# Kernel tuning notes

Measured on AMD Instinct MI355X. Metric: run time of the kernel, lower is better.

The kernel has to match this reference:

```python
import jax, jax.numpy as jnp
import numpy as np

E = 128  # embed_size


def setup_inputs() -> dict:
    key = jax.random.key(0)
    ks = jax.random.split(key, 20)
    NU, NI, NEV = 100000, 50000, 4096
    s = 0.05  # weight scale so softplus(dot) stays well-conditioned
    inp = {
        "user_emb": jax.random.normal(ks[0], (NU, E), jnp.float32) * s,
        "item_emb": jax.random.normal(ks[1], (NI, E), jnp.float32) * s,
        "ugru_wi": jax.random.normal(ks[2], (3 * E, E), jnp.float32) * s,
        "ugru_wh": jax.random.normal(ks[3], (3 * E, E), jnp.float32) * s,
        "ugru_bi": jax.random.normal(ks[4], (3 * E,), jnp.float32) * s,
        "ugru_bh": jax.random.normal(ks[5], (3 * E,), jnp.float32) * s,
        "igru_wi": jax.random.normal(ks[6], (3 * E, E), jnp.float32) * s,
        "igru_wh": jax.random.normal(ks[7], (3 * E, E), jnp.float32) * s,
        "igru_bi": jax.random.normal(ks[8], (3 * E,), jnp.float32) * s,
        "igru_bh": jax.random.normal(ks[9], (3 * E,), jnp.float32) * s,
        "t1_w": jax.random.normal(ks[10], (E, 2 * E), jnp.float32) * s,
        "t1_b": jax.random.normal(ks[11], (E,), jnp.float32) * s,
        "t2_w": jax.random.normal(ks[12], (32, E), jnp.float32) * s,
        "t2_b": jax.random.normal(ks[13], (32,), jnp.float32) * s,
        "t3_w": jax.random.normal(ks[14], (1, 32), jnp.float32) * s,
        "t3_b": jax.random.normal(ks[15], (1,), jnp.float32) * s,
        "user_ids": jax.random.randint(ks[16], (NEV,), 0, NU, jnp.int32),
        "item_ids": jax.random.randint(ks[17], (NEV,), 0, NI, jnp.int32),
    }
    return inp


def _gru(x, h, wi, wh, bi, bh):
    # torch.nn.GRUCell math, single sample: x,h [E]; wi,wh [3E,E]
    gi = wi @ x + bi
    gh = wh @ h + bh
    ir, iz, inn = jnp.split(gi, 3)
    hr, hz, hn = jnp.split(gh, 3)
    r = jax.nn.sigmoid(ir + hr)
    z = jax.nn.sigmoid(iz + hz)
    n = jnp.tanh(inn + r * hn)
    return (1.0 - z) * n + z * h


def reference(user_emb, item_emb, ugru_wi, ugru_wh, ugru_bi, ugru_bh,
              igru_wi, igru_wh, igru_bi, igru_bh,
              t1_w, t1_b, t2_w, t2_b, t3_w, t3_b,
              user_ids, item_ids):
    # Sequential event processing: per-event gather of user/item embedding,
    # Rayleigh base compatibility score, MLP (transForm1/2/3) branch score,
    # coupled GRUCell updates scattered back into the embedding tables.
    def step(carry, ev):
        U, V = carry
        u_id, i_id = ev
        u = U[u_id]          # [E] gather (dict-cache lookup in original)
        v = V[i_id]          # [E]
        comp = jax.nn.softplus(jnp.dot(u, v)) + 1e-10  # base_compatibility
        loss = -jnp.log(comp)                           # -log p(event)
        cat = jnp.concatenate([u, v])                   # [2E]
        h = jax.nn.relu(t1_w @ cat + t1_b)              # transForm1 + act
        h = jax.nn.relu(t2_w @ h + t2_b)                # transForm2 + act
        score = jax.nn.sigmoid(t3_w @ h + t3_b)[0]      # transForm3
        nu = _gru(v, u, ugru_wi, ugru_wh, ugru_bi, ugru_bh)  # user_cell
        nv = _gru(u, v, igru_wi, igru_wh, igru_bi, igru_bh)  # item_cell
        U = U.at[u_id].set(nu)  # coevolution scatter
        V = V.at[i_id].set(nv)
        return (U, V), jnp.stack([loss, score])

    (_, _), outs = jax.lax.scan(step, (user_emb, item_emb),
                                (user_ids, item_ids))
    return outs  # [num_events, 2] : (-log comp, branch score)
```

## Files before the change

kernel.cpp:

```cpp
#include <hip/hip_runtime.h>
#include <math.h>

#define EMB 128
#define MAXEV 4096

struct Hdr { int nl0; int nl1; int ncomp2; };

typedef __attribute__((ext_vector_type(8))) short bf16x8;
typedef __attribute__((ext_vector_type(4))) float f32x4;

__device__ __forceinline__ float sigmoidf_(float x) { return 1.0f / (1.0f + expf(-x)); }
__device__ __forceinline__ float softplusf_(float x) {
    return (x > 0.f) ? x + log1pf(expf(-x)) : log1pf(expf(x));
}
__device__ __forceinline__ unsigned short f2bf(float f) {
    unsigned int u = __float_as_uint(f);
    u += 0x7FFFu + ((u >> 16) & 1u);
    return (unsigned short)(u >> 16);
}

__global__ __launch_bounds__(64) void prev_kernel(
    const int* __restrict__ uids, const int* __restrict__ iids,
    int* __restrict__ prevu, int* __restrict__ previ, int nev)
{
    int t = blockIdx.x;
    if (t >= nev) return;
    int lane = threadIdx.x;
    int myu = uids[t], myi = iids[t];
    int bu = -1, bi = -1;
    for (int j = lane; j < t; j += 64) {
        if (uids[j] == myu) bu = j;
        if (iids[j] == myi) bi = j;
    }
    for (int off = 32; off; off >>= 1) {
        bu = max(bu, __shfl_xor(bu, off));
        bi = max(bi, __shfl_xor(bi, off));
    }
    if (lane == 0) { prevu[t] = bu; previ[t] = bi; }
}

__global__ __launch_bounds__(1024) void setup_kernel(
    const int* __restrict__ prevu, const int* __restrict__ previ,
    int* __restrict__ order0, int* __restrict__ order1,
    int* __restrict__ tail2Order, int* __restrict__ compStart,
    Hdr* __restrict__ hdr, int nev)
{
    __shared__ int   lab[MAXEV];
    __shared__ int   tmpT[MAXEV];
    __shared__ int   skey[MAXEV];
    __shared__ short slev[MAXEV];
    __shared__ int   schanged, sn0, sn1, sn2;

    int tid = threadIdx.x;
    for (int t = tid; t < nev; t += 1024) { lab[t] = t; slev[t] = 0; }
    if (tid == 0) { sn0 = 0; sn1 = 0; sn2 = 0; }
    __syncthreads();

    for (int it = 0; it < nev; ++it) {
        if (tid == 0) schanged = 0;
        __syncthreads();
        for (int t = tid; t < nev; t += 1024) {
            int pu = prevu[t], pi = previ[t];
            int nl = 0;
            if (pu >= 0) nl = slev[pu] + 1;
            if (pi >= 0) { int c = slev[pi] + 1; nl = nl > c ? nl : c; }
            if (nl > (int)slev[t]) { slev[t] = (short)nl; schanged = 1; }
        }
        __syncthreads();
        if (!schanged) break;
        __syncthreads();
    }

    for (int it = 0; it < nev; ++it) {
        if (tid == 0) schanged = 0;
        __syncthreads();
        for (int t = tid; t < nev; t += 1024) {
            int m = lab[t];
            int pu = prevu[t], pi = previ[t];
            if (pu >= 0) m = min(m, lab[pu]);
            if (pi >= 0) m = min(m, lab[pi]);
            if (m < lab[t]) { atomicMin(&lab[t], m); schanged = 1; }
            if (pu >= 0 && m < lab[pu]) { atomicMin(&lab[pu], m); schanged = 1; }
            if (pi >= 0 && m < lab[pi]) { atomicMin(&lab[pi], m); schanged = 1; }
        }
        __syncthreads();
        if (!schanged) break;
        __syncthreads();
    }

    for (int t = tid; t < nev; t += 1024) {
        int l = slev[t];
        if (l == 0)      order0[atomicAdd(&sn0, 1)] = t;
        else if (l == 1) order1[atomicAdd(&sn1, 1)] = t;
        else             tmpT[atomicAdd(&sn2, 1)] = t;
    }
    __syncthreads();
    int n2 = sn2;

    for (int i = tid; i < n2; i += 1024)
        skey[i] = (lab[tmpT[i]] << 12) | tmpT[i];
    __syncthreads();

    for (int i = tid; i < n2; i += 1024) {
        int k = skey[i], r = 0;
        for (int j = 0; j < n2; ++j) r += (skey[j] < k);
        tail2Order[r] = tmpT[i];
        lab[r] = k;
    }
    __syncthreads();

    if (tid == 0) {
        int nc = 0;
        for (int i = 0; i < n2; ++i)
            if (i == 0 || (lab[i] >> 12) != (lab[i - 1] >> 12))
                compStart[nc++] = i;
        compStart[nc] = n2;
        hdr->nl0 = sn0;
        hdr->nl1 = sn1;
        hdr->ncomp2 = nc;
    }
}

__global__ __launch_bounds__(256) void wcvt_kernel(
    const float* __restrict__ Wuh, const float* __restrict__ Wii,
    const float* __restrict__ Wui, const float* __restrict__ Wih,
    const float* __restrict__ T1w,
    unsigned short* __restrict__ wb_uh, unsigned short* __restrict__ wb_ii,
    unsigned short* __restrict__ wb_ui, unsigned short* __restrict__ wb_ih,
    unsigned short* __restrict__ t1wb)
{
    int m = blockIdx.y;
    const float* src = (m == 0) ? Wuh : (m == 1) ? Wii : (m == 2) ? Wui
                      : (m == 3) ? Wih : T1w;
    unsigned short* dst = (m == 0) ? wb_uh : (m == 1) ? wb_ii : (m == 2) ? wb_ui
                        : (m == 3) ? wb_ih : t1wb;
    int nf4 = (m < 4) ? (384 * EMB / 4) : (EMB * 256 / 4);
    int q = blockIdx.x * 256 + threadIdx.x;
    if (q >= nf4) return;
    float4 v = ((const float4*)src)[q];
    ushort4 o = make_ushort4(f2bf(v.x), f2bf(v.y), f2bf(v.z), f2bf(v.w));
    *(ushort4*)(dst + (size_t)q * 4) = o;
}

__global__ __launch_bounds__(256) void gatherx_kernel(
    const float* __restrict__ U0, const float* __restrict__ V0,
    const int* __restrict__ uids, const int* __restrict__ iids,
    const int* __restrict__ prevu, const int* __restrict__ previ,
    const float* __restrict__ NU, const float* __restrict__ NV,
    const int* __restrict__ order, const int* __restrict__ cnt_p,
    float* __restrict__ Xu, float* __restrict__ Xv,
    unsigned short* __restrict__ Xub, unsigned short* __restrict__ Xvb)
{
    int cnt = *cnt_p;
    int NP64 = (cnt + 63) & ~63;
    int sub = threadIdx.x >> 5;
    int lane = threadIdx.x & 31;
    int e = blockIdx.x * 8 + sub;
    if (e >= NP64) return;
    float4 a, c;
    if (e < cnt) {
        int t = order[e];
        int pu = prevu[t], pi = previ[t];
        const float4* up = (const float4*)(pu < 0 ?
            U0 + (size_t)uids[t] * EMB : NU + (size_t)pu * EMB);
        const float4* vp = (const float4*)(pi < 0 ?
            V0 + (size_t)iids[t] * EMB : NV + (size_t)pi * EMB);
        a = up[lane];
        c = vp[lane];
    } else {
        a = make_float4(0.f, 0.f, 0.f, 0.f);
        c = a;
    }
    ((float4*)(Xu + (size_t)e * EMB))[lane] = a;
    ((float4*)(Xv + (size_t)e * EMB))[lane] = c;
    *(ushort4*)(Xub + (size_t)e * EMB + lane * 4) =
        make_ushort4(f2bf(a.x), f2bf(a.y), f2bf(a.z), f2bf(a.w));
    *(ushort4*)(Xvb + (size_t)e * EMB + lane * 4) =
        make_ushort4(f2bf(c.x), f2bf(c.y), f2bf(c.z), f2bf(c.w));
}

__global__ __launch_bounds__(256) void gate_mfma_kernel(
    const unsigned short* __restrict__ Xub, const unsigned short* __restrict__ Xvb,
    const unsigned short* __restrict__ wb_uh, const unsigned short* __restrict__ wb_ii,
    const unsigned short* __restrict__ wb_ui, const unsigned short* __restrict__ wb_ih,
    const int* __restrict__ cnt_p,
    float* __restrict__ Gu, float* __restrict__ Gv)
{
    int cnt = *cnt_p;
    int NP64 = (cnt + 63) & ~63;
    int ev0 = blockIdx.x * 64;
    if (ev0 >= NP64) return;
    int z = blockIdx.z;
    int j = blockIdx.y;
    const unsigned short* X  = z ? Xvb : Xub;
    const unsigned short* W1 = z ? wb_ui : wb_uh;
    const unsigned short* W2 = z ? wb_ih : wb_ii;
    float* G = z ? Gv : Gu;
    const unsigned short* Wsrc = (j < 6) ? W1 : W2;
    int row0 = ((j < 6) ? j : j - 6) * 64;

    int tid = threadIdx.x;
    int w = tid >> 6, l = tid & 63;
    int lr = l & 15, lk = (l >> 4) * 8;

    const unsigned short* xp = X + (size_t)(ev0 + w * 16 + lr) * EMB + lk;
    const unsigned short* wp = Wsrc + (size_t)(row0 + lr) * EMB + lk;

    f32x4 acc[4] = {};
    #pragma unroll
    for (int kk = 0; kk < 4; ++kk) {
        bf16x8 a = *(const bf16x8*)(xp + kk * 32);
        #pragma unroll
        for (int n = 0; n < 4; ++n) {
            bf16x8 b = *(const bf16x8*)(wp + (size_t)n * 16 * EMB + kk * 32);
            acc[n] = __builtin_amdgcn_mfma_f32_16x16x32_bf16(a, b, acc[n], 0, 0, 0);
        }
    }
    int drow = ev0 + w * 16 + (l >> 4) * 4;
    int col = j * 64 + lr;
    #pragma unroll
    for (int n = 0; n < 4; ++n) {
        #pragma unroll
        for (int i = 0; i < 4; ++i)
            G[(size_t)(drow + i) * 768 + col + n * 16] = acc[n][i];
    }
}

__global__ __launch_bounds__(256) void combine_kernel(
    const float* __restrict__ Gu, const float* __restrict__ Gv,
    const float* __restrict__ Xu, const float* __restrict__ Xv,
    const float* __restrict__ bui, const float* __restrict__ buh,
    const float* __restrict__ bii, const float* __restrict__ bih,
    const int* __restrict__ order, const int* __restrict__ cnt_p,
    float* __restrict__ NU, float* __restrict__ NV)
{
    int cnt = *cnt_p;
    int e = blockIdx.x * 2 + (threadIdx.x >> 7);
    int rr = threadIdx.x & 127;
    if (e >= cnt) return;
    int t = order[e];
    const float* gu = Gu + (size_t)e * 768;
    const float* gv = Gv + (size_t)e * 768;
    float r = sigmoidf_(gv[rr] + bui[rr] + gu[rr] + buh[rr]);
    float zg = sigmoidf_(gv[128 + rr] + bui[128 + rr] + gu[128 + rr] + buh[128 + rr]);
    float n = tanhf(gv[256 + rr] + bui[256 + rr] + r * (gu[256 + rr] + buh[256 + rr]));
    float u = Xu[(size_t)e * EMB + rr];
    NU[(size_t)t * EMB + rr] = (1.f - zg) * n + zg * u;
    float r2 = sigmoidf_(gu[384 + rr] + bii[rr] + gv[384 + rr] + bih[rr]);
    float z2 = sigmoidf_(gu[512 + rr] + bii[128 + rr] + gv[512 + rr] + bih[128 + rr]);
    float n2 = tanhf(gu[640 + rr] + bii[256 + rr] + r2 * (gv[640 + rr] + bih[256 + rr]));
    float v = Xv[(size_t)e * EMB + rr];
    NV[(size_t)t * EMB + rr] = (1.f - z2) * n2 + z2 * v;
}

__global__ __launch_bounds__(1024) void tail2_kernel(
    const float* __restrict__ U0,  const float* __restrict__ V0,
    const float* __restrict__ Wui, const float* __restrict__ Wuh,
    const float* __restrict__ bui, const float* __restrict__ buh,
    const float* __restrict__ Wii, const float* __restrict__ Wih,
    const float* __restrict__ bii, const float* __restrict__ bih,
    const int* __restrict__ uids,  const int* __restrict__ iids,
    const int* __restrict__ prevu, const int* __restrict__ previ,
    const int* __restrict__ tail2Order, const int* __restrict__ compStart,
    const Hdr* __restrict__ hdr,
    float* __restrict__ NU, float* __restrict__ NV)
{
    __shared__ __align__(16) float su[EMB];
    __shared__ __align__(16) float sv[EMB];
    __shared__ float gg[1536];
    int tid = threadIdx.x;
    int ncomp = hdr->ncomp2;

    int g = tid >> 4, j = tid & 15;
    int mat = g >> 4;
    const float* W = (mat == 0) ? Wui : (mat == 1) ? Wuh : (mat == 2) ? Wii : Wih;

    for (int c = blockIdx.x; c < ncomp; c += gridDim.x) {
        int kb = compStart[c], ke = compStart[c + 1];
        for (int k = kb; k < ke; ++k) {
            int t = tail2Order[k];
            int pu = prevu[t], pi = previ[t];
            const float* up = (pu < 0) ? U0 + (size_t)uids[t] * EMB : NU + (size_t)pu * EMB;
            const float* vp = (pi < 0) ? V0 + (size_t)iids[t] * EMB : NV + (size_t)pi * EMB;
            __syncthreads();
            if (tid < EMB)        su[tid] = up[tid];
            else if (tid < 2*EMB) sv[tid - EMB] = vp[tid - EMB];
            __syncthreads();

            const float* x = (mat == 1 || mat == 2) ? su : sv;
            const float4* x4 = (const float4*)x;
            float4 xa = x4[2 * j], xb = x4[2 * j + 1];
            #pragma unroll 1
            for (int b = 0; b < 3; ++b) {
                int rbase = (g & 15) * 24 + b * 8;
                float4 w0[8], w1[8];
                #pragma unroll
                for (int q = 0; q < 8; ++q) {
                    const float4* W4 = (const float4*)(W + (size_t)(rbase + q) * EMB);
                    w0[q] = W4[2 * j]; w1[q] = W4[2 * j + 1];
                }
                #pragma unroll
                for (int q = 0; q < 8; ++q) {
                    float s = w0[q].x * xa.x + w0[q].y * xa.y
                            + w0[q].z * xa.z + w0[q].w * xa.w
                            + w1[q].x * xb.x + w1[q].y * xb.y
                            + w1[q].z * xb.z + w1[q].w * xb.w;
                    s += __shfl_xor(s, 1); s += __shfl_xor(s, 2);
                    s += __shfl_xor(s, 4); s += __shfl_xor(s, 8);
                    if (j == q) gg[mat * 384 + rbase + q] = s;
                }
            }
            __syncthreads();

            if (tid < EMB) {
                int e = tid;
                float r_ = sigmoidf_(gg[e] + bui[e] + gg[384 + e] + buh[e]);
                float z_ = sigmoidf_(gg[128 + e] + bui[128 + e] + gg[512 + e] + buh[128 + e]);
                float n_ = tanhf(gg[256 + e] + bui[256 + e] + r_ * (gg[640 + e] + buh[256 + e]));
                NU[(size_t)t * EMB + e] = (1.f - z_) * n_ + z_ * su[e];
            } else if (tid < 2*EMB) {
                int e = tid - EMB;
                float r_ = sigmoidf_(gg[768 + e] + bii[e] + gg[1152 + e] + bih[e]);
                float z_ = sigmoidf_(gg[896 + e] + bii[128 + e] + gg[1280 + e] + bih[128 + e]);
                float n_ = tanhf(gg[1024 + e] + bii[256 + e] + r_ * (gg[1408 + e] + bih[256 + e]));
                NV[(size_t)t * EMB + e] = (1.f - z_) * n_ + z_ * sv[e];
            }
        }
    }
}

__global__ __launch_bounds__(256) void gatherall_kernel(
    const float* __restrict__ U0, const float* __restrict__ V0,
    const int* __restrict__ uids, const int* __restrict__ iids,
    const int* __restrict__ prevu, const int* __restrict__ previ,
    const float* __restrict__ NU, const float* __restrict__ NV,
    unsigned short* __restrict__ XAub, unsigned short* __restrict__ XAvb,
    float* __restrict__ out, int nev)
{
    int sub = threadIdx.x >> 5;
    int lane = threadIdx.x & 31;
    int t = blockIdx.x * 8 + sub;
    if (t >= nev) return;
    int pu = prevu[t], pi = previ[t];
    const float4* up = (const float4*)(pu < 0 ?
        U0 + (size_t)uids[t] * EMB : NU + (size_t)pu * EMB);
    const float4* vp = (const float4*)(pi < 0 ?
        V0 + (size_t)iids[t] * EMB : NV + (size_t)pi * EMB);
    float4 a = up[lane], c = vp[lane];
    *(ushort4*)(XAub + (size_t)t * EMB + lane * 4) =
        make_ushort4(f2bf(a.x), f2bf(a.y), f2bf(a.z), f2bf(a.w));
    *(ushort4*)(XAvb + (size_t)t * EMB + lane * 4) =
        make_ushort4(f2bf(c.x), f2bf(c.y), f2bf(c.z), f2bf(c.w));
    float dp = a.x * c.x + a.y * c.y + a.z * c.z + a.w * c.w;
    dp += __shfl_xor(dp, 1); dp += __shfl_xor(dp, 2);
    dp += __shfl_xor(dp, 4); dp += __shfl_xor(dp, 8);
    dp += __shfl_xor(dp, 16);
    if (lane == 0) out[2 * (size_t)t] = -logf(softplusf_(dp) + 1e-10f);
}

__global__ __launch_bounds__(256) void t1_mfma_kernel(
    const unsigned short* __restrict__ XAub, const unsigned short* __restrict__ XAvb,
    const unsigned short* __restrict__ t1wb, const float* __restrict__ T1b,
    float* __restrict__ H1, int nev)
{
    int ev0 = blockIdx.x * 64;
    int row0 = blockIdx.y * 64;
    int tid = threadIdx.x;
    int w = tid >> 6, l = tid & 63;
    int lr = l & 15, lk = (l >> 4) * 8;
    int erow = ev0 + w * 16 + lr;

    f32x4 acc[4] = {};
    #pragma unroll
    for (int kh = 0; kh < 8; ++kh) {
        const unsigned short* Xb = (kh < 4) ? XAub : XAvb;
        bf16x8 a = *(const bf16x8*)(Xb + (size_t)erow * EMB + (kh & 3) * 32 + lk);
        #pragma unroll
        for (int n = 0; n < 4; ++n) {
            bf16x8 b = *(const bf16x8*)(t1wb + (size_t)(row0 + n * 16 + lr) * 256 + kh * 32 + lk);
            acc[n] = __builtin_amdgcn_mfma_f32_16x16x32_bf16(a, b, acc[n], 0, 0, 0);
        }
    }
    int drow = ev0 + w * 16 + (l >> 4) * 4;
    #pragma unroll
    for (int n = 0; n < 4; ++n) {
        int col = row0 + n * 16 + lr;
        float bb = T1b[col];
        #pragma unroll
        for (int i = 0; i < 4; ++i)
            H1[(size_t)(drow + i) * EMB + col] = fmaxf(acc[n][i] + bb, 0.f);
    }
}

__global__ __launch_bounds__(256) void t2t3_kernel(
    const float* __restrict__ H1,
    const float* __restrict__ T2w, const float* __restrict__ T2b,
    const float* __restrict__ T3w, const float* __restrict__ T3b,
    float* __restrict__ out, int nev)
{
    __shared__ __align__(16) float w2s[32][132];
    __shared__ __align__(16) float h1s[16][132];
    __shared__ float h2s[16][36];
    int tid = threadIdx.x;
    int ev = tid >> 4, j = tid & 15;
    int t = blockIdx.x * 16 + ev;

    {
        const float4* s2 = (const float4*)T2w;
        #pragma unroll
        for (int i = 0; i < 4; ++i) {
            int q = i * 256 + tid;
            int r = q >> 5, c4 = q & 31;
            *(float4*)&w2s[r][c4 * 4] = s2[q];
        }
    }
    {
        const float4* h4 = (const float4*)(H1 + (size_t)(blockIdx.x * 16 + ev) * EMB);
        *(float4*)&h1s[ev][8 * j]     = h4[2 * j];
        *(float4*)&h1s[ev][8 * j + 4] = h4[2 * j + 1];
    }
    __syncthreads();

    float acc0 = T2b[2 * j], acc1 = T2b[2 * j + 1];
    const float4* wr0 = (const float4*)&w2s[2 * j][0];
    const float4* wr1 = (const float4*)&w2s[2 * j + 1][0];
    const float4* xh = (const float4*)&h1s[ev][0];
    #pragma unroll
    for (int k = 0; k < 32; ++k) {
        float4 x = xh[k], a = wr0[k], b = wr1[k];
        acc0 = fmaf(a.x, x.x, acc0); acc0 = fmaf(a.y, x.y, acc0);
        acc0 = fmaf(a.z, x.z, acc0); acc0 = fmaf(a.w, x.w, acc0);
        acc1 = fmaf(b.x, x.x, acc1); acc1 = fmaf(b.y, x.y, acc1);
        acc1 = fmaf(b.z, x.z, acc1); acc1 = fmaf(b.w, x.w, acc1);
    }
    h2s[ev][2 * j]     = fmaxf(acc0, 0.f);
    h2s[ev][2 * j + 1] = fmaxf(acc1, 0.f);
    __syncthreads();

    float p = T3w[2 * j] * h2s[ev][2 * j] + T3w[2 * j + 1] * h2s[ev][2 * j + 1];
    p += __shfl_xor(p, 1); p += __shfl_xor(p, 2);
    p += __shfl_xor(p, 4); p += __shfl_xor(p, 8);
    if (j == 0 && t < nev)
        out[2 * (size_t)t + 1] = sigmoidf_(p + T3b[0]);
}

extern "C" void kernel_launch(void* const* d_in, const int* in_sizes, int n_in,
                              void* d_out, int out_size, void* d_ws, size_t ws_size,
                              hipStream_t stream)
{
    const float* U0  = (const float*)d_in[0];
    const float* V0  = (const float*)d_in[1];
    const float* Wui = (const float*)d_in[2];
    const float* Wuh = (const float*)d_in[3];
    const float* bui = (const float*)d_in[4];
    const float* buh = (const float*)d_in[5];
    const float* Wii = (const float*)d_in[6];
    const float* Wih = (const float*)d_in[7];
    const float* bii = (const float*)d_in[8];
    const float* bih = (const float*)d_in[9];
    const float* T1w = (const float*)d_in[10];
    const float* T1b = (const float*)d_in[11];
    const float* T2w = (const float*)d_in[12];
    const float* T2b = (const float*)d_in[13];
    const float* T3w = (const float*)d_in[14];
    const float* T3b = (const float*)d_in[15];
    const int* uids  = (const int*)d_in[16];
    const int* iids  = (const int*)d_in[17];
    int nev = in_sizes[16];

    char* ws = (char*)d_ws;
    int* base = (int*)ws;
    int* prevu      = base;
    int* previ      = base + MAXEV;
    int* order0     = base + 2 * MAXEV;
    int* order1     = base + 3 * MAXEV;
    int* tail2Order = base + 4 * MAXEV;
    int* compStart  = base + 5 * MAXEV;
    Hdr* hdr        = (Hdr*)(base + 6 * MAXEV + 4);
    float* NU = (float*)(ws + (160 << 10));
    float* NV = NU + (size_t)MAXEV * EMB;
    float* Xu = NV + (size_t)MAXEV * EMB;
    float* Xv = Xu + (size_t)MAXEV * EMB;
    float* Gu = Xv + (size_t)MAXEV * EMB;
    float* Gv = Gu + (size_t)MAXEV * 768;
    unsigned short* Xub = (unsigned short*)(Gv + (size_t)MAXEV * 768);
    unsigned short* Xvb = Xub + (size_t)MAXEV * EMB;
    unsigned short* wb_uh = Xvb + (size_t)MAXEV * EMB;
    unsigned short* wb_ii = wb_uh + 384 * EMB;
    unsigned short* wb_ui = wb_ii + 384 * EMB;
    unsigned short* wb_ih = wb_ui + 384 * EMB;
    unsigned short* t1wb  = wb_ih + 384 * EMB;
    float* out = (float*)d_out;

    prev_kernel<<<nev, 64, 0, stream>>>(uids, iids, prevu, previ, nev);
    wcvt_kernel<<<dim3(48, 5), 256, 0, stream>>>(
        Wuh, Wii, Wui, Wih, T1w, wb_uh, wb_ii, wb_ui, wb_ih, t1wb);
    setup_kernel<<<1, 1024, 0, stream>>>(prevu, previ, order0, order1,
                                         tail2Order, compStart, hdr, nev);

    gatherx_kernel<<<(MAXEV + 7) / 8, 256, 0, stream>>>(
        U0, V0, uids, iids, prevu, previ, NU, NV, order0, &hdr->nl0,
        Xu, Xv, Xub, Xvb);
    gate_mfma_kernel<<<dim3(MAXEV / 64, 12, 2), 256, 0, stream>>>(
        Xub, Xvb, wb_uh, wb_ii, wb_ui, wb_ih, &hdr->nl0, Gu, Gv);
    combine_kernel<<<(MAXEV + 1) / 2, 256, 0, stream>>>(
        Gu, Gv, Xu, Xv, bui, buh, bii, bih, order0, &hdr->nl0, NU, NV);

    gatherx_kernel<<<(MAXEV + 7) / 8, 256, 0, stream>>>(
        U0, V0, uids, iids, prevu, previ, NU, NV, order1, &hdr->nl1,
        Xu, Xv, Xub, Xvb);
    gate_mfma_kernel<<<dim3(MAXEV / 64, 12, 2), 256, 0, stream>>>(
        Xub, Xvb, wb_uh, wb_ii, wb_ui, wb_ih, &hdr->nl1, Gu, Gv);
    combine_kernel<<<(MAXEV + 1) / 2, 256, 0, stream>>>(
        Gu, Gv, Xu, Xv, bui, buh, bii, bih, order1, &hdr->nl1, NU, NV);

    tail2_kernel<<<64, 1024, 0, stream>>>(
        U0, V0, Wui, Wuh, bui, buh, Wii, Wih, bii, bih,
        uids, iids, prevu, previ, tail2Order, compStart, hdr, NU, NV);

    unsigned short* XAub = Xub;
    unsigned short* XAvb = Xvb;
    float* H1 = Gu;
    gatherall_kernel<<<(nev + 7) / 8, 256, 0, stream>>>(
        U0, V0, uids, iids, prevu, previ, NU, NV, XAub, XAvb, out, nev);
    t1_mfma_kernel<<<dim3((nev + 63) / 64, 2), 256, 0, stream>>>(
        XAub, XAvb, t1wb, T1b, H1, nev);
    t2t3_kernel<<<(nev + 15) / 16, 256, 0, stream>>>(
        H1, T2w, T2b, T3w, T3b, out, nev);
}
```

Before: 127.1 us.

## Fuse gather, GRU gate MFMA and combine into one kernel per level

Replaces the three-kernel gather / bf16 MFMA gate GEMM / combine sequence with a single kernel per dependency level. Each block processes 16 events: it stages their bf16 inputs in shared memory, computes all gate outputs with MFMA into shared memory, and applies the GRU nonlinearity directly. This removes intermediate global buffers and four kernel launches. In exchange, each block rereads the full weight matrices for only 16 events, and the hidden state used in the final blend is now the bf16-rounded value instead of fp32.

```diff
diff --git a/kernel.cpp b/kernel.cpp
--- a/kernel.cpp
+++ b/kernel.cpp
@@ -3,6 +3,7 @@
 
 #define EMB 128
 #define MAXEV 4096
+#define GEV 16
 
 struct Hdr { int nl0; int nl1; int ncomp2; };
 
@@ -17,6 +18,9 @@
     unsigned int u = __float_as_uint(f);
     u += 0x7FFFu + ((u >> 16) & 1u);
     return (unsigned short)(u >> 16);
+}
+__device__ __forceinline__ float bf2f(unsigned short s) {
+    return __uint_as_float((unsigned int)s << 16);
 }
 
 __global__ __launch_bounds__(64) void prev_kernel(
@@ -142,115 +146,103 @@
     *(ushort4*)(dst + (size_t)q * 4) = o;
 }
 
-__global__ __launch_bounds__(256) void gatherx_kernel(
+__global__ __launch_bounds__(256) void gru_fused_kernel(
     const float* __restrict__ U0, const float* __restrict__ V0,
+    const unsigned short* __restrict__ wb_ui, const unsigned short* __restrict__ wb_uh,
+    const unsigned short* __restrict__ wb_ii, const unsigned short* __restrict__ wb_ih,
+    const float* __restrict__ bui, const float* __restrict__ buh,
+    const float* __restrict__ bii, const float* __restrict__ bih,
     const int* __restrict__ uids, const int* __restrict__ iids,
     const int* __restrict__ prevu, const int* __restrict__ previ,
-    const float* __restrict__ NU, const float* __restrict__ NV,
+    const float* NUr, const float* NVr,
     const int* __restrict__ order, const int* __restrict__ cnt_p,
-    float* __restrict__ Xu, float* __restrict__ Xv,
-    unsigned short* __restrict__ Xub, unsigned short* __restrict__ Xvb)
-{
+    float* NU, float* NV)
+{
+    __shared__ __align__(16) unsigned short xbu[GEV][EMB];
+    __shared__ __align__(16) unsigned short xbv[GEV][EMB];
+    __shared__ float gg[GEV][772];
+
     int cnt = *cnt_p;
-    int NP64 = (cnt + 63) & ~63;
-    int sub = threadIdx.x >> 5;
-    int lane = threadIdx.x & 31;
-    int e = blockIdx.x * 8 + sub;
-    if (e >= NP64) return;
-    float4 a, c;
-    if (e < cnt) {
-        int t = order[e];
-        int pu = prevu[t], pi = previ[t];
-        const float4* up = (const float4*)(pu < 0 ?
-            U0 + (size_t)uids[t] * EMB : NU + (size_t)pu * EMB);
-        const float4* vp = (const float4*)(pi < 0 ?
-            V0 + (size_t)iids[t] * EMB : NV + (size_t)pi * EMB);
-        a = up[lane];
-        c = vp[lane];
-    } else {
-        a = make_float4(0.f, 0.f, 0.f, 0.f);
-        c = a;
-    }
-    ((float4*)(Xu + (size_t)e * EMB))[lane] = a;
-    ((float4*)(Xv + (size_t)e * EMB))[lane] = c;
-    *(ushort4*)(Xub + (size_t)e * EMB + lane * 4) =
-        make_ushort4(f2bf(a.x), f2bf(a.y), f2bf(a.z), f2bf(a.w));
-    *(ushort4*)(Xvb + (size_t)e * EMB + lane * 4) =
-        make_ushort4(f2bf(c.x), f2bf(c.y), f2bf(c.z), f2bf(c.w));
-}
-
-__global__ __launch_bounds__(256) void gate_mfma_kernel(
-    const unsigned short* __restrict__ Xub, const unsigned short* __restrict__ Xvb,
-    const unsigned short* __restrict__ wb_uh, const unsigned short* __restrict__ wb_ii,
-    const unsigned short* __restrict__ wb_ui, const unsigned short* __restrict__ wb_ih,
-    const int* __restrict__ cnt_p,
-    float* __restrict__ Gu, float* __restrict__ Gv)
-{
-    int cnt = *cnt_p;
-    int NP64 = (cnt + 63) & ~63;
-    int ev0 = blockIdx.x * 64;
-    if (ev0 >= NP64) return;
-    int z = blockIdx.z;
-    int j = blockIdx.y;
-    const unsigned short* X  = z ? Xvb : Xub;
-    const unsigned short* W1 = z ? wb_ui : wb_uh;
-    const unsigned short* W2 = z ? wb_ih : wb_ii;
-    float* G = z ? Gv : Gu;
-    const unsigned short* Wsrc = (j < 6) ? W1 : W2;
-    int row0 = ((j < 6) ? j : j - 6) * 64;
+    int e0 = blockIdx.x * GEV;
+    if (e0 >= cnt) return;
 
     int tid = threadIdx.x;
+    int ev = tid >> 4, c8 = (tid & 15) * 8;
+
+    {
+        int e = e0 + ev;
+        float4 a0, a1, c0, c1;
+        if (e < cnt) {
+            int t = order[e];
+            int pu = prevu[t], pi = previ[t];
+            const float* up = (pu < 0 ? U0 + (size_t)uids[t] * EMB : NUr + (size_t)pu * EMB) + c8;
+            const float* vp = (pi < 0 ? V0 + (size_t)iids[t] * EMB : NVr + (size_t)pi * EMB) + c8;
+            a0 = ((const float4*)up)[0]; a1 = ((const float4*)up)[1];
+            c0 = ((const float4*)vp)[0]; c1 = ((const float4*)vp)[1];
+        } else {
+            a0 = make_float4(0.f, 0.f, 0.f, 0.f); a1 = a0; c0 = a0; c1 = a0;
+        }
+        *(ushort4*)&xbu[ev][c8]     = make_ushort4(f2bf(a0.x), f2bf(a0.y), f2bf(a0.z), f2bf(a0.w));
+        *(ushort4*)&xbu[ev][c8 + 4] = make_ushort4(f2bf(a1.x), f2bf(a1.y), f2bf(a1.z), f2bf(a1.w));
+        *(ushort4*)&xbv[ev][c8]     = make_ushort4(f2bf(c0.x), f2bf(c0.y), f2bf(c0.z), f2bf(c0.w));
+        *(ushort4*)&xbv[ev][c8 + 4] = make_ushort4(f2bf(c1.x), f2bf(c1.y), f2bf(c1.z), f2bf(c1.w));
+    }
+    __syncthreads();
+
     int w = tid >> 6, l = tid & 63;
     int lr = l & 15, lk = (l >> 4) * 8;
 
-    const unsigned short* xp = X + (size_t)(ev0 + w * 16 + lr) * EMB + lk;
-    const unsigned short* wp = Wsrc + (size_t)(row0 + lr) * EMB + lk;
-
-    f32x4 acc[4] = {};
-    #pragma unroll
-    for (int kk = 0; kk < 4; ++kk) {
-        bf16x8 a = *(const bf16x8*)(xp + kk * 32);
+    for (int ph = 0; ph < 2; ++ph) {
+        const unsigned short* Wi = ph ? wb_ii : wb_ui;
+        const unsigned short* Wh = ph ? wb_ih : wb_uh;
+        const unsigned short (*Xi)[EMB] = ph ? xbu : xbv;
+        const unsigned short (*Xh)[EMB] = ph ? xbv : xbu;
+
+        f32x4 acc[12] = {};
         #pragma unroll
-        for (int n = 0; n < 4; ++n) {
-            bf16x8 b = *(const bf16x8*)(wp + (size_t)n * 16 * EMB + kk * 32);
-            acc[n] = __builtin_amdgcn_mfma_f32_16x16x32_bf16(a, b, acc[n], 0, 0, 0);
-        }
-    }
-    int drow = ev0 + w * 16 + (l >> 4) * 4;
-    int col = j * 64 + lr;
-    #pragma unroll
-    for (int n = 0; n < 4; ++n) {
+        for (int kk = 0; kk < 4; ++kk) {
+            bf16x8 ai = *(const bf16x8*)&Xi[lr][kk * 32 + lk];
+            bf16x8 ah = *(const bf16x8*)&Xh[lr][kk * 32 + lk];
+            #pragma unroll
+            for (int j = 0; j < 12; ++j) {
+                int nt = w * 12 + j;
+                bool ish = nt >= 24;
+                int brow = (ish ? nt - 24 : nt) * 16 + lr;
+                const unsigned short* W = ish ? Wh : Wi;
+                bf16x8 b = *(const bf16x8*)(W + (size_t)brow * EMB + kk * 32 + lk);
+                acc[j] = __builtin_amdgcn_mfma_f32_16x16x32_bf16(ish ? ah : ai, b, acc[j], 0, 0, 0);
+            }
+        }
         #pragma unroll
-        for (int i = 0; i < 4; ++i)
-            G[(size_t)(drow + i) * 768 + col + n * 16] = acc[n][i];
-    }
-}
-
-__global__ __launch_bounds__(256) void combine_kernel(
-    const float* __restrict__ Gu, const float* __restrict__ Gv,
-    const float* __restrict__ Xu, const float* __restrict__ Xv,
-    const float* __restrict__ bui, const float* __restrict__ buh,
-    const float* __restrict__ bii, const float* __restrict__ bih,
-    const int* __restrict__ order, const int* __restrict__ cnt_p,
-    float* __restrict__ NU, float* __restrict__ NV)
-{
-    int cnt = *cnt_p;
-    int e = blockIdx.x * 2 + (threadIdx.x >> 7);
-    int rr = threadIdx.x & 127;
-    if (e >= cnt) return;
-    int t = order[e];
-    const float* gu = Gu + (size_t)e * 768;
-    const float* gv = Gv + (size_t)e * 768;
-    float r = sigmoidf_(gv[rr] + bui[rr] + gu[rr] + buh[rr]);
-    float zg = sigmoidf_(gv[128 + rr] + bui[128 + rr] + gu[128 + rr] + buh[128 + rr]);
-    float n = tanhf(gv[256 + rr] + bui[256 + rr] + r * (gu[256 + rr] + buh[256 + rr]));
-    float u = Xu[(size_t)e * EMB + rr];
-    NU[(size_t)t * EMB + rr] = (1.f - zg) * n + zg * u;
-    float r2 = sigmoidf_(gu[384 + rr] + bii[rr] + gv[384 + rr] + bih[rr]);
-    float z2 = sigmoidf_(gu[512 + rr] + bii[128 + rr] + gv[512 + rr] + bih[128 + rr]);
-    float n2 = tanhf(gu[640 + rr] + bii[256 + rr] + r2 * (gv[640 + rr] + bih[256 + rr]));
-    float v = Xv[(size_t)e * EMB + rr];
-    NV[(size_t)t * EMB + rr] = (1.f - z2) * n2 + z2 * v;
+        for (int j = 0; j < 12; ++j) {
+            int nt = w * 12 + j;
+            #pragma unroll
+            for (int i = 0; i < 4; ++i)
+                gg[(l >> 4) * 4 + i][nt * 16 + lr] = acc[j][i];
+        }
+        __syncthreads();
+
+        {
+            int e = e0 + ev;
+            if (e < cnt) {
+                int t = order[e];
+                const float* bi = ph ? bii : bui;
+                const float* bh = ph ? bih : buh;
+                float* N = ph ? NV : NU;
+                const unsigned short (*xh)[EMB] = ph ? xbv : xbu;
+                #pragma unroll
+                for (int i = 0; i < 8; ++i) {
+                    int ch = c8 + i;
+                    float r_ = sigmoidf_(gg[ev][ch] + bi[ch] + gg[ev][384 + ch] + bh[ch]);
+                    float z_ = sigmoidf_(gg[ev][128 + ch] + bi[128 + ch] + gg[ev][512 + ch] + bh[128 + ch]);
+                    float n_ = tanhf(gg[ev][256 + ch] + bi[256 + ch] + r_ * (gg[ev][640 + ch] + bh[256 + ch]));
+                    float h = bf2f(xh[ev][ch]);
+                    N[(size_t)t * EMB + ch] = (1.f - z_) * n_ + z_ * h;
+                }
+            }
+        }
+        __syncthreads();
+    }
 }
 
 __global__ __launch_bounds__(1024) void tail2_kernel(
@@ -498,21 +490,13 @@
     setup_kernel<<<1, 1024, 0, stream>>>(prevu, previ, order0, order1,
                                          tail2Order, compStart, hdr, nev);
 
-    gatherx_kernel<<<(MAXEV + 7) / 8, 256, 0, stream>>>(
-        U0, V0, uids, iids, prevu, previ, NU, NV, order0, &hdr->nl0,
-        Xu, Xv, Xub, Xvb);
-    gate_mfma_kernel<<<dim3(MAXEV / 64, 12, 2), 256, 0, stream>>>(
-        Xub, Xvb, wb_uh, wb_ii, wb_ui, wb_ih, &hdr->nl0, Gu, Gv);
-    combine_kernel<<<(MAXEV + 1) / 2, 256, 0, stream>>>(
-        Gu, Gv, Xu, Xv, bui, buh, bii, bih, order0, &hdr->nl0, NU, NV);
-
-    gatherx_kernel<<<(MAXEV + 7) / 8, 256, 0, stream>>>(
-        U0, V0, uids, iids, prevu, previ, NU, NV, order1, &hdr->nl1,
-        Xu, Xv, Xub, Xvb);
-    gate_mfma_kernel<<<dim3(MAXEV / 64, 12, 2), 256, 0, stream>>>(
-        Xub, Xvb, wb_uh, wb_ii, wb_ui, wb_ih, &hdr->nl1, Gu, Gv);
-    combine_kernel<<<(MAXEV + 1) / 2, 256, 0, stream>>>(
-        Gu, Gv, Xu, Xv, bui, buh, bii, bih, order1, &hdr->nl1, NU, NV);
+    gru_fused_kernel<<<MAXEV / GEV, 256, 0, stream>>>(
+        U0, V0, wb_ui, wb_uh, wb_ii, wb_ih, bui, buh, bii, bih,
+        uids, iids, prevu, previ, NU, NV, order0, &hdr->nl0, NU, NV);
+
+    gru_fused_kernel<<<MAXEV / GEV, 256, 0, stream>>>(
+        U0, V0, wb_ui, wb_uh, wb_ii, wb_ih, bui, buh, bii, bih,
+        uids, iids, prevu, previ, NU, NV, order1, &hdr->nl1, NU, NV);
 
     tail2_kernel<<<64, 1024, 0, stream>>>(
         U0, V0, Wui, Wuh, bui, buh, Wii, Wih, bii, bih,
```

Result: faster. 122.6 us (-3.6%).
